# Kernel optimization log

Measured on AMD Instinct MI355X. Metric: run time of the kernel, lower is better.

Reference implementation:

```python
import jax, jax.numpy as jnp
import numpy as np
import math

TEMP = 0.07
BASE_TEMP = 0.07
M = 0.2
S = 10.0
COS_M = math.cos(M)
SIN_M = math.sin(M)
TH = math.cos(math.pi - M)
MM = math.sin(math.pi - M) * M
N_CLASSES = 2793
EPS = 1e-12


def _l2norm_rows(x):
    # F.normalize(x, p=2, dim=1)
    n = jnp.linalg.norm(x, axis=1, keepdims=True)
    return x / jnp.maximum(n, EPS)


def setup_inputs() -> dict:
    key = jax.random.key(0)
    k1, k2, k3, k4 = jax.random.split(key, 4)
    bsz, n_views, d = 1024, 2, 192
    return {
        "features": jax.random.normal(k1, (bsz, n_views, d), jnp.float32),
        "labels": jax.random.randint(k2, (bsz,), 0, N_CLASSES),
        "fc_w": jax.random.normal(k3, (N_CLASSES, d), jnp.float32) * 0.05,
        "fc_b": jax.random.normal(k4, (N_CLASSES,), jnp.float32) * 0.01,
    }


def reference(features, labels, fc_w, fc_b):
    bsz, n_views, d = features.shape
    n = bsz * n_views  # 2048 (must be <= N_CLASSES for the one_hot scatter)

    # supervised mask from labels: mask[i,j] = 1 if same class
    mask = (labels[:, None] == labels[None, :]).astype(jnp.float32)  # [bsz,bsz]

    # contrast_feature = cat(unbind(features, dim=1), dim=0), then L2-normalized
    cf = jnp.concatenate([features[:, v] for v in range(n_views)], axis=0)  # [n,d]
    cf = _l2norm_rows(cf)
    anchor = cf  # contrast_mode == 'all'

    x_norm = jnp.maximum(jnp.linalg.norm(cf, axis=1, keepdims=True), 1e-12)
    x = cf / x_norm
    w_norm = jnp.maximum(jnp.linalg.norm(anchor, axis=1, keepdims=True), 1e-12)
    w = anchor / w_norm

    cosine = x @ w.T                      # [n,n]
    cosine = _l2norm_rows(cosine)         # row L2-normalize (as in source)
    sine = jnp.sqrt(jnp.clip(1.0 - cosine * cosine, 0.0, 1.0))
    phi = cosine * COS_M - sine * SIN_M
    phi = jnp.where(cosine - TH > 0, phi, cosine - MM)
    output = S * phi                      # [n,n]

    attlabels = jnp.concatenate([labels, labels])  # [n]

    # h2 @ one_hot where one_hot[j,k] = 1 iff j < n and attlabels[j] == k
    # => (h2 @ one_hot)[i,k] = sum_{j<n, attlabels[j]==k} h2[i,j]
    h2 = jnp.tanh(cf @ fc_w.T + fc_b)     # [n, N_CLASSES]
    seg = jax.ops.segment_sum(h2[:, :n].T, attlabels, num_segments=N_CLASSES)  # [C,n]
    denominator = jnp.exp(seg.T)          # [n, N_CLASSES]; zero cols -> exp(0)=1

    # vectorized form of per-row python loop: a_i = den[i, attlabels[i]] / sum(den[i])
    num = jnp.take_along_axis(denominator, attlabels[:, None], axis=1)[:, 0]  # [n]
    a = num / denominator.sum(axis=1)     # [n]
    # F.normalize on [n,1]: each row divided by its own |a| -> sign(a) (here all 1)
    atten = a / jnp.maximum(jnp.abs(a), EPS)  # [n]
    # A = min(expand(atten), expand(atten)) == atten broadcast along rows
    A = atten[:, None]                    # [n,1], broadcasts over columns

    anchor_dot_contrast = output / TEMP
    logits_max = jax.lax.stop_gradient(anchor_dot_contrast.max(axis=1, keepdims=True))
    logits = (anchor_dot_contrast - logits_max) * A

    mask_full = jnp.tile(mask, (n_views, n_views))            # [n,n]
    logits_mask = 1.0 - jnp.eye(n, dtype=jnp.float32)          # zero diagonal
    mask_full = mask_full * logits_mask

    exp_logits = jnp.exp(logits) * logits_mask
    log_prob = logits - jnp.log(exp_logits.sum(axis=1, keepdims=True))
    mean_log_prob_pos = (mask_full * log_prob).sum(axis=1) / mask_full.sum(axis=1)

    loss = -(TEMP / BASE_TEMP) * mean_log_prob_pos
    return loss.reshape(n_views, bsz).mean()
```

## Files before the change

### kernel.cpp

```cpp
#include <hip/hip_runtime.h>

typedef __attribute__((ext_vector_type(8))) _Float16 half8;
typedef __attribute__((ext_vector_type(4))) float f32x4;

#define COS_M 0.98006657784124163f
#define SIN_M 0.19866933079506122f
#define TH_C  (-0.98006657784124163f)
#define MM_C  0.039733866159012244f
#define S_OVER_TEMP (10.0f / 0.07f)

__device__ inline float xform(float c) {
  float s2 = fmaxf(1.0f - c * c, 0.0f);
  float sn = sqrtf(s2);
  float phi = c * COS_M - sn * SIN_M;
  float out = (c - TH_C > 0.0f) ? phi : (c - MM_C);
  return out * S_OVER_TEMP;
}

__global__ __launch_bounds__(64) void k_normalize(const float* __restrict__ feats,
                                                  _Float16* __restrict__ cfn) {
  const int i = blockIdx.x;
  const int b = i & 1023, v = i >> 10;
  const float* src = feats + ((size_t)b * 2 + v) * 192;
  const int t = threadIdx.x;
  float x0 = src[t], x1 = src[t + 64], x2 = src[t + 128];
  float ss = x0 * x0 + x1 * x1 + x2 * x2;
#pragma unroll
  for (int o = 32; o; o >>= 1) ss += __shfl_down(ss, o);
  ss = __shfl(ss, 0);
  float inv = 1.0f / fmaxf(sqrtf(ss), 1e-12f);
  _Float16* dst = cfn + (size_t)i * 192;
  dst[t]       = (_Float16)(x0 * inv);
  dst[t + 64]  = (_Float16)(x1 * inv);
  dst[t + 128] = (_Float16)(x2 * inv);
}

__global__ __launch_bounds__(256) void k_gemm(const _Float16* __restrict__ cfn,
                                              _Float16* __restrict__ Gh) {
  __shared__ alignas(16) _Float16 la[128 * 200];
  __shared__ alignas(16) _Float16 lb[128 * 200];
  const int bm = blockIdx.x, bn = blockIdx.y;
  const uint4* srcA = (const uint4*)(cfn + (size_t)bm * 128 * 192);
  const uint4* srcB = (const uint4*)(cfn + (size_t)bn * 128 * 192);
  for (int idx = threadIdx.x; idx < 3072; idx += 256) {
    int r = idx / 24, c = idx - r * 24;
    *(uint4*)&la[r * 200 + c * 8] = srcA[idx];
    *(uint4*)&lb[r * 200 + c * 8] = srcB[idx];
  }
  __syncthreads();

  const int lane = threadIdx.x & 63;
  const int w = threadIdx.x >> 6;
  const int wr = w >> 1, wc = w & 1;
  const int lr = lane & 15, kg = lane >> 4;

  f32x4 acc[4][4];
#pragma unroll
  for (int m = 0; m < 4; ++m)
#pragma unroll
    for (int n = 0; n < 4; ++n) acc[m][n] = (f32x4){0.f, 0.f, 0.f, 0.f};

#pragma unroll
  for (int kc = 0; kc < 6; ++kc) {
    half8 af[4], bf[4];
    const int koff = kc * 32 + kg * 8;
#pragma unroll
    for (int m = 0; m < 4; ++m)
      af[m] = *(const half8*)&la[(wr * 64 + m * 16 + lr) * 200 + koff];
#pragma unroll
    for (int n = 0; n < 4; ++n)
      bf[n] = *(const half8*)&lb[(wc * 64 + n * 16 + lr) * 200 + koff];
#pragma unroll
    for (int m = 0; m < 4; ++m)
#pragma unroll
      for (int n = 0; n < 4; ++n)
        acc[m][n] = __builtin_amdgcn_mfma_f32_16x16x32_f16(af[m], bf[n], acc[m][n], 0, 0, 0);
  }

  const int rb = bm * 128 + wr * 64;
  const int cb = bn * 128 + wc * 64;
#pragma unroll
  for (int m = 0; m < 4; ++m)
#pragma unroll
    for (int n = 0; n < 4; ++n) {
      const int r0 = rb + m * 16 + kg * 4;
      const int c0 = cb + n * 16 + lr;
#pragma unroll
      for (int e = 0; e < 4; ++e)
        Gh[(size_t)(r0 + e) * 2048 + c0] = (_Float16)acc[m][n][e];
    }
}

__global__ __launch_bounds__(64) void k_rowloss(const _Float16* __restrict__ Gh,
                                                const int* __restrict__ labels,
                                                float* __restrict__ lossv) {
  const int i = blockIdx.x;
  const int l = threadIdx.x;
  const _Float16* row = Gh + (size_t)i * 2048;

  half8 v[4];
#pragma unroll
  for (int p = 0; p < 4; ++p)
    v[p] = *(const half8*)&row[512 * p + 8 * l];

  float gv[4][8];
#pragma unroll
  for (int p = 0; p < 4; ++p)
#pragma unroll
    for (int u = 0; u < 8; ++u) gv[p][u] = (float)v[p][u];

  float ss = 0.f, mx = -3.4e38f;
#pragma unroll
  for (int p = 0; p < 4; ++p)
#pragma unroll
    for (int u = 0; u < 8; ++u) { ss += gv[p][u] * gv[p][u]; mx = fmaxf(mx, gv[p][u]); }
#pragma unroll
  for (int o = 32; o; o >>= 1) {
    ss += __shfl_xor(ss, o);
    mx = fmaxf(mx, __shfl_xor(mx, o));
  }
  const float invn = 1.0f / fmaxf(sqrtf(ss), 1e-12f);
  const float Mst = xform(mx * invn);

  const int4 a0 = *(const int4*)&labels[8 * l];
  const int4 a1 = *(const int4*)&labels[8 * l + 4];
  const int4 b0 = *(const int4*)&labels[512 + 8 * l];
  const int4 b1 = *(const int4*)&labels[512 + 8 * l + 4];
  const int labs[2][8] = {{a0.x, a0.y, a0.z, a0.w, a1.x, a1.y, a1.z, a1.w},
                          {b0.x, b0.y, b0.z, b0.w, b1.x, b1.y, b1.z, b1.w}};
  const int mylab = labels[i & 1023];

  float es = 0.f, ps = 0.f, cn = 0.f;
#pragma unroll
  for (int p = 0; p < 4; ++p)
#pragma unroll
    for (int u = 0; u < 8; ++u) {
      const int j = 512 * p + 8 * l + u;
      const float lg = xform(gv[p][u] * invn) - Mst;
      if (j != i) {
        es += expf(lg);
        if (labs[p & 1][u] == mylab) { ps += lg; cn += 1.f; }
      }
    }
#pragma unroll
  for (int o = 32; o; o >>= 1) {
    es += __shfl_xor(es, o);
    ps += __shfl_xor(ps, o);
    cn += __shfl_xor(cn, o);
  }
  if (l == 0) lossv[i] = -(ps / cn - logf(es));
}

__global__ __launch_bounds__(256) void k_final(const float* __restrict__ lossv,
                                               float* __restrict__ out) {
  const int t = threadIdx.x;
  float s = 0.f;
  for (int j = t; j < 2048; j += 256) s += lossv[j];
#pragma unroll
  for (int o = 32; o; o >>= 1) s += __shfl_down(s, o);
  __shared__ float r4[4];
  if ((t & 63) == 0) r4[t >> 6] = s;
  __syncthreads();
  if (t == 0) out[0] = (r4[0] + r4[1] + r4[2] + r4[3]) * (1.0f / 2048.0f);
}

extern "C" void kernel_launch(void* const* d_in, const int* in_sizes, int n_in,
                              void* d_out, int out_size, void* d_ws, size_t ws_size,
                              hipStream_t stream) {
  const float* feats = (const float*)d_in[0];
  const int* labels = (const int*)d_in[1];

  char* ws = (char*)d_ws;
  float* lossv  = (float*)ws;
  _Float16* cfn = (_Float16*)(ws + 16384);
  _Float16* Gh  = (_Float16*)(ws + (1 << 20));

  k_normalize<<<2048, 64, 0, stream>>>(feats, cfn);
  dim3 g2(16, 16);
  k_gemm<<<g2, 256, 0, stream>>>(cfn, Gh);
  k_rowloss<<<2048, 64, 0, stream>>>(Gh, labels, lossv);
  k_final<<<1, 256, 0, stream>>>(lossv, (float*)d_out);
}
```

Measured before the change: 31.55 us.

## Fuse row L2-normalization into GEMM by scaling outputs with inverse norms

Removes the separate normalize kernel. Each GEMM block now loads fp32 features directly, converts them to fp16 in LDS and computes per-row inverse norms. The dot products are rescaled by both row scales in the epilogue. Diagonal blocks reuse the A tile for B. This saves one launch and the intermediate round trip, at the cost of redundant fp32 reads across blocks and fp16 quantization of unnormalized values.

```diff
diff --git a/kernel.cpp b/kernel.cpp
--- a/kernel.cpp
+++ b/kernel.cpp
@@ -17,40 +17,42 @@
   return out * S_OVER_TEMP;
 }
 
-__global__ __launch_bounds__(64) void k_normalize(const float* __restrict__ feats,
-                                                  _Float16* __restrict__ cfn) {
-  const int i = blockIdx.x;
-  const int b = i & 1023, v = i >> 10;
-  const float* src = feats + ((size_t)b * 2 + v) * 192;
-  const int t = threadIdx.x;
-  float x0 = src[t], x1 = src[t + 64], x2 = src[t + 128];
-  float ss = x0 * x0 + x1 * x1 + x2 * x2;
-#pragma unroll
-  for (int o = 32; o; o >>= 1) ss += __shfl_down(ss, o);
-  ss = __shfl(ss, 0);
-  float inv = 1.0f / fmaxf(sqrtf(ss), 1e-12f);
-  _Float16* dst = cfn + (size_t)i * 192;
-  dst[t]       = (_Float16)(x0 * inv);
-  dst[t + 64]  = (_Float16)(x1 * inv);
-  dst[t + 128] = (_Float16)(x2 * inv);
-}
-
-__global__ __launch_bounds__(256) void k_gemm(const _Float16* __restrict__ cfn,
-                                              _Float16* __restrict__ Gh) {
+__global__ __launch_bounds__(256) void k_gemm_norm(const float* __restrict__ feats,
+                                                   _Float16* __restrict__ Gh) {
   __shared__ alignas(16) _Float16 la[128 * 200];
   __shared__ alignas(16) _Float16 lb[128 * 200];
+  __shared__ float rsA[128], rsBs[128];
   const int bm = blockIdx.x, bn = blockIdx.y;
-  const uint4* srcA = (const uint4*)(cfn + (size_t)bm * 128 * 192);
-  const uint4* srcB = (const uint4*)(cfn + (size_t)bn * 128 * 192);
-  for (int idx = threadIdx.x; idx < 3072; idx += 256) {
-    int r = idx / 24, c = idx - r * 24;
-    *(uint4*)&la[r * 200 + c * 8] = srcA[idx];
-    *(uint4*)&lb[r * 200 + c * 8] = srcB[idx];
-  }
+  const int t = threadIdx.x;
+  const bool diag = (bn == bm);
+
+  auto stage = [&](int bt, _Float16* lds, float* rs) {
+    const int rr = t >> 1, h = t & 1;
+    const int r = bt * 128 + rr;
+    const float4* s4 =
+        (const float4*)(feats + (size_t)((r & 1023) * 2 + (r >> 10)) * 192 + h * 96);
+    float ss = 0.f;
+    _Float16* dst = lds + rr * 200 + h * 96;
+#pragma unroll
+    for (int q = 0; q < 12; ++q) {
+      float4 va = s4[2 * q], vb = s4[2 * q + 1];
+      ss += va.x * va.x + va.y * va.y + va.z * va.z + va.w * va.w;
+      ss += vb.x * vb.x + vb.y * vb.y + vb.z * vb.z + vb.w * vb.w;
+      half8 o = {(_Float16)va.x, (_Float16)va.y, (_Float16)va.z, (_Float16)va.w,
+                 (_Float16)vb.x, (_Float16)vb.y, (_Float16)vb.z, (_Float16)vb.w};
+      *(half8*)(dst + q * 8) = o;
+    }
+    ss += __shfl_xor(ss, 1);
+    if (h == 0) rs[rr] = rsqrtf(fmaxf(ss, 1e-24f));
+  };
+  stage(bm, la, rsA);
+  if (!diag) stage(bn, lb, rsBs);
   __syncthreads();
+  const _Float16* Bp = diag ? la : lb;
+  const float* rsB = diag ? rsA : rsBs;
 
-  const int lane = threadIdx.x & 63;
-  const int w = threadIdx.x >> 6;
+  const int lane = t & 63;
+  const int w = t >> 6;
   const int wr = w >> 1, wc = w & 1;
   const int lr = lane & 15, kg = lane >> 4;
 
@@ -69,7 +71,7 @@
       af[m] = *(const half8*)&la[(wr * 64 + m * 16 + lr) * 200 + koff];
 #pragma unroll
     for (int n = 0; n < 4; ++n)
-      bf[n] = *(const half8*)&lb[(wc * 64 + n * 16 + lr) * 200 + koff];
+      bf[n] = *(const half8*)&Bp[(wc * 64 + n * 16 + lr) * 200 + koff];
 #pragma unroll
     for (int m = 0; m < 4; ++m)
 #pragma unroll
@@ -85,9 +87,12 @@
     for (int n = 0; n < 4; ++n) {
       const int r0 = rb + m * 16 + kg * 4;
       const int c0 = cb + n * 16 + lr;
+      const float sb = rsB[wc * 64 + n * 16 + lr];
 #pragma unroll
-      for (int e = 0; e < 4; ++e)
-        Gh[(size_t)(r0 + e) * 2048 + c0] = (_Float16)acc[m][n][e];
+      for (int e = 0; e < 4; ++e) {
+        const float sa = rsA[wr * 64 + m * 16 + kg * 4 + e];
+        Gh[(size_t)(r0 + e) * 2048 + c0] = (_Float16)(acc[m][n][e] * sa * sb);
+      }
     }
 }
 
@@ -171,13 +176,11 @@
   const int* labels = (const int*)d_in[1];
 
   char* ws = (char*)d_ws;
-  float* lossv  = (float*)ws;
-  _Float16* cfn = (_Float16*)(ws + 16384);
-  _Float16* Gh  = (_Float16*)(ws + (1 << 20));
+  float* lossv = (float*)ws;
+  _Float16* Gh = (_Float16*)(ws + (1 << 20));
 
-  k_normalize<<<2048, 64, 0, stream>>>(feats, cfn);
   dim3 g2(16, 16);
-  k_gemm<<<g2, 256, 0, stream>>>(cfn, Gh);
+  k_gemm_norm<<<g2, 256, 0, stream>>>(feats, Gh);
   k_rowloss<<<2048, 64, 0, stream>>>(Gh, labels, lossv);
   k_final<<<1, 256, 0, stream>>>(lossv, (float*)d_out);
 }
```

Measured after the change: 29.13 us. 7.7% less time.
